# Kernel tuning notes

Hardware: AMD Instinct MI355X
Metric: run time of the kernel (lower is better)

The kernel has to match this reference:

```python
import jax, jax.numpy as jnp
import numpy as np


def _gen_grid(h, w, stride=1):
    """Normalized spherical sampling grid, shape (3*H', 3*W', 2) with (x, y) order,
    matching gen_grid_coordinates in the torch source (vectorized)."""
    pi = np.pi
    dphi = pi / h
    dth = 2 * pi / w
    t = np.tan(dth)
    p = np.tan(dphi)
    sp = p / np.cos(dth)
    # xys[kr, kc] = (x, y) tangent-plane offsets of the 3x3 kernel taps
    xys = np.array([[[-t, sp], [0.0, p], [t, sp]],
                    [[-t, 0.0], [1.0, 1.0], [t, 0.0]],
                    [[-t, -sp], [0.0, -p], [t, -sp]]], dtype=np.float64)
    X = xys[..., 0]
    Y = xys[..., 1]
    rho = np.sqrt(X ** 2 + Y ** 2)           # [3,3], nonzero everywhere
    v = np.arctan(rho)
    rr = np.arange(0, h, stride)
    cc = np.arange(0, w, stride)
    phi = -((rr + 0.5) / h * pi - pi / 2)    # [H']
    theta = (cc + 0.5) / w * 2 * pi - pi     # [W']
    sphi = np.sin(phi)[:, None, None, None]  # [H',1,1,1]
    cphi = np.cos(phi)[:, None, None, None]
    arg = np.cos(v) * sphi + Y * np.sin(v) * cphi / rho  # [H',1,3,3]
    new_phi = np.arcsin(np.clip(arg, -1.0, 1.0))
    new_theta = theta[None, :, None, None] + np.arctan(
        X * np.sin(v) / (rho * cphi * np.cos(v) - Y * sphi * np.sin(v)))  # [H',W',3,3]
    new_r = np.broadcast_to((-new_phi + pi / 2) * h / pi - 0.5, new_theta.shape).copy()
    new_c = (new_theta + pi) * w / (2 * pi) - 0.5
    new_c = (new_c + w) % w
    # center tap samples the pixel itself
    new_r[:, :, 1, 1] = rr[:, None]
    new_c[:, :, 1, 1] = cc[None, :]
    gx = new_c * 2 / w - 1
    gy = new_r * 2 / h - 1
    grid = np.stack([gx, gy], axis=-1)                     # [H',W',3,3,2]
    Hp, Wp = len(rr), len(cc)
    grid = grid.transpose(0, 2, 1, 3, 4).reshape(Hp * 3, Wp * 3, 2)
    return grid.astype(np.float32)


def _grid_sample_bilinear_zeros(x, grid):
    """torch grid_sample(mode='bilinear', padding_mode='zeros', align_corners=False).
    x: [N,C,H,W]; grid: [Hg,Wg,2] (shared over batch). Returns [N,C,Hg,Wg]."""
    N, C, H, W = x.shape
    ix = ((grid[..., 0] + 1) * W - 1) * 0.5
    iy = ((grid[..., 1] + 1) * H - 1) * 0.5
    x0 = jnp.floor(ix)
    y0 = jnp.floor(iy)
    x1 = x0 + 1
    y1 = y0 + 1
    wx1 = ix - x0
    wx0 = 1.0 - wx1
    wy1 = iy - y0
    wy0 = 1.0 - wy1

    def gather(yy, xx):
        valid = ((xx >= 0) & (xx <= W - 1) & (yy >= 0) & (yy <= H - 1)).astype(x.dtype)
        xi = jnp.clip(xx, 0, W - 1).astype(jnp.int32)
        yi = jnp.clip(yy, 0, H - 1).astype(jnp.int32)
        return x[:, :, yi, xi], valid  # [N,C,Hg,Wg], [Hg,Wg]

    v00, m00 = gather(y0, x0)
    v01, m01 = gather(y0, x1)
    v10, m10 = gather(y1, x0)
    v11, m11 = gather(y1, x1)
    return (v00 * (wy0 * wx0 * m00) + v01 * (wy0 * wx1 * m01)
            + v10 * (wy1 * wx0 * m10) + v11 * (wy1 * wx1 * m11))


def setup_inputs() -> dict:
    key = jax.random.key(0)
    k1, k2, k3 = jax.random.split(key, 3)
    N, Cin, H, W = 4, 64, 128, 256
    Cout = 128
    x = jax.random.normal(k1, (N, Cin, H, W), dtype=jnp.float32)
    fan_in = Cin * 9
    bound = 1.0 / np.sqrt(fan_in)
    weight = jax.random.uniform(k2, (Cout, Cin, 3, 3), dtype=jnp.float32,
                                minval=-bound, maxval=bound)
    bias = jnp.zeros((Cout,), dtype=jnp.float32)
    return {"x": x, "weight": weight, "bias": bias}


def reference(x, weight, bias):
    H, W = int(x.shape[2]), int(x.shape[3])
    grid = jnp.asarray(_gen_grid(H, W, 1))              # [3H, 3W, 2]
    s = _grid_sample_bilinear_zeros(x, grid)            # [N, Cin, 3H, 3W]
    y = jax.lax.conv_general_dilated(
        s, weight, window_strides=(3, 3), padding='VALID',
        dimension_numbers=('NCHW', 'OIHW', 'NCHW'))     # [N, Cout, H, W]
    return y + bias[None, :, None, None]
```

## Files before the change

### kernel.cpp

```cpp
#include <hip/hip_runtime.h>
#include <math.h>

typedef __attribute__((ext_vector_type(8))) short short8;
typedef __attribute__((ext_vector_type(8))) _Float16 half8;
typedef __attribute__((ext_vector_type(4))) _Float16 half4;
typedef __attribute__((ext_vector_type(2))) _Float16 half2;
typedef __attribute__((ext_vector_type(4))) float floatx4;
typedef __attribute__((ext_vector_type(4))) unsigned int uintx4;

#define NB    4
#define CIN   64
#define COUT  128
#define IMH   128
#define IMW   256
#define KTOT  576
#define NPIX  (IMH * IMW)
#define PXT   128
#define NDPB  (PXT * 9)
#define ROWS  4
#define CSTW  6
#define NCOL  257
#define RSTW  (NCOL * CSTW)
#define SLSTR 104
#define KCH   96

__device__ __forceinline__ unsigned pkrtz2(float a, float b) {
  unsigned r;
  asm("v_cvt_pkrtz_f16_f32 %0, %1, %2" : "=v"(r) : "v"(a), "v"(b));
  return r;
}
__device__ __forceinline__ half4 dup4(unsigned u) {
  half2 h; __builtin_memcpy(&h, &u, 4);
  return __builtin_shufflevector(h, h, 0, 1, 0, 1);
}

__global__ __launch_bounds__(256) void prep_w_kernel(const float* __restrict__ w,
                                                     unsigned short* __restrict__ wbf) {
  int idx = blockIdx.x * 256 + threadIdx.x;
  if (idx >= COUT * 8 * KCH) return;
  int co = idx / (8 * KCH);
  int K2 = idx - co * (8 * KCH);
  int cb = K2 / KCH, kk = K2 - cb * KCH;
  unsigned short v = 0;
  if (kk < 72) {
    int t = kk >> 3, chl = kk & 7;
    int ci = cb * 8 + chl;
    _Float16 h = (_Float16)w[co * KTOT + ci * 9 + t];
    __builtin_memcpy(&v, &h, 2);
  }
  wbf[(K2 >> 3) * (COUT * 8) + co * 8 + (K2 & 7)] = v;
}

__global__ __launch_bounds__(512, 4) void sphconv_kernel(
    const float* __restrict__ x, const unsigned short* __restrict__ wbf,
    const float* __restrict__ bias, float* __restrict__ out) {
  __shared__ __align__(16) unsigned int stg[ROWS * RSTW];
  __shared__ __align__(16) unsigned short Sl[PXT * SLSTR];
  __shared__ double tapA[9];
  __shared__ float  tapWy[9][2];
  __shared__ int    tapRo[9][2];

  const int tid  = threadIdx.x;
  const int lane = tid & 63;
  const int wv   = tid >> 6;
  const int lin = blockIdx.x + 2 * blockIdx.y;
  const int sw  = (lin & 7) * 32 + (lin >> 3);
  const int ct  = sw >> 7;
  const int r   = sw & 127;
  const int n   = blockIdx.z;
  const int c0  = ct * PXT;
  const int co_base = (wv & 1) * 64;
  const int px_base = (wv >> 1) * 32;
  const int rlo  = min(max(r - 2, 0), IMH - ROWS);
  const int sp  = tid & 3;
  const int scg = (tid >> 2) & 63;
  const int srr = tid >> 8;

  const float* xn = x + (size_t)n * CIN * NPIX;

  floatx4 nx[4];
  #pragma unroll
  for (int c = 0; c < 2; c++)
    #pragma unroll
    for (int rw = 0; rw < 2; rw++)
      nx[c * 2 + rw] = *(const floatx4*)(xn + (size_t)(sp * 2 + c) * NPIX
                                         + (size_t)(rlo + srr * 2 + rw) * IMW + scg * 4);

  {
    int myk = -1;
    if (lane == 0) myk = wv;
    if (wv == 0 && lane == 32) myk = 8;
    if (myk >= 0) {
      const double pi = 3.14159265358979323846;
      double dphi = pi / IMH;
      double dth  = 2.0 * pi / IMW;
      double t  = tan(dth);
      double p  = tan(dphi);
      double sp_ = p / cos(dth);
      double phi  = -(((double)r + 0.5) / IMH * pi - pi * 0.5);
      double sphi = sin(phi), cphi = cos(phi);
      int i = myk / 3, j = myk % 3;
      double atv, new_r;
      if (myk == 4) {
        atv = 0.0; new_r = (double)r;
      } else {
        double X = (j == 0) ? -t : ((j == 2) ? t : 0.0);
        double Y = 0.0;
        if (i == 0)      Y = (j == 1) ?  p :  sp_;
        else if (i == 2) Y = (j == 1) ? -p : -sp_;
        double rho = sqrt(X * X + Y * Y);
        double v   = atan(rho);
        double sv = sin(v), cv = cos(v);
        double arg = cv * sphi + Y * sv * cphi / rho;
        arg = fmin(1.0, fmax(-1.0, arg));
        double new_phi = asin(arg);
        double denom = rho * cphi * cv - Y * sphi * sv;
        atv = atan(X * sv / denom);
        new_r = (-new_phi + pi * 0.5) * IMH / pi - 0.5;
      }
      float gy = (float)(new_r * 2.0 / IMH - 1.0);
      float iy = ((gy + 1.0f) * (float)IMH - 1.0f) * 0.5f;
      float fy = floorf(iy); int y0 = (int)fy;
      float wy1 = iy - fy, wy0 = 1.0f - wy1;
      int y1 = y0 + 1;
      bool vy0 = (y0 >= 0) & (y0 <= IMH - 1);
      bool vy1 = (y1 >= 0) & (y1 <= IMH - 1);
      int y0c = min(max(y0, 0), IMH - 1), y1c = min(max(y1, 0), IMH - 1);
      int rt = min(max(y0c - rlo, 0), ROWS - 1);
      int rb = min(max(y1c - rlo, 0), ROWS - 1);
      tapA[myk] = atv;
      tapWy[myk][0] = vy0 ? wy0 : 0.0f;
      tapWy[myk][1] = vy1 ? wy1 : 0.0f;
      tapRo[myk][0] = rt * RSTW;
      tapRo[myk][1] = rb * RSTW;
    }
  }
  __syncthreads();

  int opk[3] = {0, 0, 0}, slw[3] = {0, 0, 0};
  unsigned uq0[3] = {0,0,0}, uq1[3] = {0,0,0}, uq2[3] = {0,0,0}, uq3[3] = {0,0,0};
  {
    const double pi = 3.14159265358979323846;
    #pragma unroll
    for (int dd = 0; dd < 3; dd++) {
      if (dd < 2 || tid < NDPB - 1024) {
        int d  = tid + dd * 512;
        int px = d & (PXT - 1), k = d >> 7;
        int c  = c0 + px;
        double nc;
        if (k == 4) {
          nc = (double)c;
        } else {
          double theta = ((double)c + 0.5) / IMW * (2.0 * pi) - pi;
          double new_theta = theta + tapA[k];
          nc = (new_theta + pi) * IMW / (2.0 * pi) - 0.5;
          nc = fmod(nc + (double)IMW, (double)IMW);
        }
        float gx = (float)(nc * 2.0 / IMW - 1.0);
        float ix = ((gx + 1.0f) * (float)IMW - 1.0f) * 0.5f;
        float fx = floorf(ix); int x0 = (int)fx;
        float wx1 = ix - fx, wx0 = 1.0f - wx1;
        int x1 = x0 + 1;
        int x0c = max(x0, 0);
        float w_lo = (x0 >= 0) ? wx0 : wx1;
        float w_hi = (x0 >= 0) ? ((x1 <= IMW - 1) ? wx1 : 0.0f) : 0.0f;
        float wy0m = tapWy[k][0], wy1m = tapWy[k][1];
        float w0 = wy0m * w_lo, w1 = wy0m * w_hi;
        float w2 = wy1m * w_lo, w3 = wy1m * w_hi;
        int sh0 = ((x0c >> 4) & 1) * 2;
        int sh1 = (((x0c + 1) >> 4) & 1) * 2;
        int dc  = CSTW + sh1 - sh0;
        int offt = tapRo[k][0] + x0c * CSTW + sh0;
        int offb = tapRo[k][1] + x0c * CSTW + sh0;
        opk[dd] = offt | (offb << 16);
        slw[dd] = (px * (SLSTR / 2) + k * 4) | (dc << 16);
        uq0[dd] = pkrtz2(w0, w0); uq1[dd] = pkrtz2(w1, w1);
        uq2[dd] = pkrtz2(w2, w2); uq3[dd] = pkrtz2(w3, w3);
      }
    }
  }

  #pragma unroll
  for (int rw = 0; rw < 2; rw++)
    #pragma unroll
    for (int i = 0; i < 4; i++) {
      int col = scg * 4 + i;
      int sh = ((col >> 4) & 1) * 2;
      stg[(srr * 2 + rw) * RSTW + col * CSTW + sh + sp] =
          pkrtz2(nx[rw][i], nx[2 + rw][i]);
    }
  if (tid < 16) stg[(tid >> 2) * RSTW + 256 * CSTW + (tid & 3)] = 0u;
  #pragma unroll
  for (int z = 0; z < 3; z++) {
    int q = tid + z * 512;
    int px = q / 12;
    ((unsigned int*)Sl)[px * 52 + 36 + (q - px * 12)] = 0u;
  }

  floatx4 acc[4][2];
  #pragma unroll
  for (int mt = 0; mt < 4; mt++)
    #pragma unroll
    for (int nt = 0; nt < 2; nt++)
      acc[mt][nt] = (floatx4){0.f, 0.f, 0.f, 0.f};

  __syncthreads();

  #pragma unroll 1
  for (int cb = 0; cb < 8; cb++) {
    if (cb < 7) {
      #pragma unroll
      for (int c = 0; c < 2; c++)
        #pragma unroll
        for (int rw = 0; rw < 2; rw++)
          nx[c * 2 + rw] = *(const floatx4*)(xn + (size_t)((cb + 1) * 8 + sp * 2 + c) * NPIX
                                             + (size_t)(rlo + srr * 2 + rw) * IMW + scg * 4);
    }
    #pragma unroll
    for (int dd = 0; dd < 3; dd++) {
      if (dd < 2 || tid < NDPB - 1024) {
        unsigned op = (unsigned)opk[dd];
        const unsigned* pt = stg + (op & 0xFFFFu);
        const unsigned* pb = stg + (op >> 16);
        int dc = slw[dd] >> 16;
        half4 t0  = *(const half4*)(pt);
        half4 t0h = *(const half4*)(pt + 2);
        half4 t1  = *(const half4*)(pt + dc);
        half4 t1h = *(const half4*)(pt + dc + 2);
        half4 b0  = *(const half4*)(pb);
        half4 b0h = *(const half4*)(pb + 2);
        half4 b1  = *(const half4*)(pb + dc);
        half4 b1h = *(const half4*)(pb + dc + 2);
        half4 W0 = dup4(uq0[dd]), W1 = dup4(uq1[dd]);
        half4 W2 = dup4(uq2[dd]), W3 = dup4(uq3[dd]);
        half4 slo = t0 * W0 + t1 * W1 + b0 * W2 + b1 * W3;
        half4 shi = t0h * W0 + t1h * W1 + b0h * W2 + b1h * W3;
        union { half4 h; unsigned u[2]; } ua, ub;
        ua.h = slo; ub.h = shi;
        uintx4 U = {ua.u[0], ua.u[1], ub.u[0], ub.u[1]};
        *(uintx4*)((unsigned int*)Sl + (slw[dd] & 0xFFFF)) = U;
      }
    }
    __syncthreads();
    if (cb < 7) {
      #pragma unroll
      for (int rw = 0; rw < 2; rw++)
        #pragma unroll
        for (int i = 0; i < 4; i++) {
          int col = scg * 4 + i;
          int sh = ((col >> 4) & 1) * 2;
          stg[(srr * 2 + rw) * RSTW + col * CSTW + sh + sp] =
              pkrtz2(nx[rw][i], nx[2 + rw][i]);
        }
    }
    __builtin_amdgcn_s_setprio(1);
    #pragma unroll
    for (int ks = 0; ks < 3; ks++) {
      const unsigned short* arow =
          wbf + (size_t)((cb * 12 + ks * 4 + (lane >> 4)) * COUT + co_base + (lane & 15)) * 8;
      #pragma unroll
      for (int nt = 0; nt < 2; nt++) {
        half8 b = *(const half8*)&Sl[(px_base + nt * 16 + (lane & 15)) * SLSTR
                                     + ks * 32 + (lane >> 4) * 8];
        #pragma unroll
        for (int mt = 0; mt < 4; mt++) {
          half8 a = *(const half8*)(arow + mt * 16 * 8);
          acc[mt][nt] = __builtin_amdgcn_mfma_f32_16x16x32_f16(a, b, acc[mt][nt], 0, 0, 0);
        }
      }
    }
    __builtin_amdgcn_s_setprio(0);
    __syncthreads();
  }

  #pragma unroll
  for (int mt = 0; mt < 4; mt++)
    #pragma unroll
    for (int nt = 0; nt < 2; nt++)
      #pragma unroll
      for (int rg = 0; rg < 4; rg++) {
        const int co = co_base + mt * 16 + (lane >> 4) * 4 + rg;
        const int cc = c0 + px_base + nt * 16 + (lane & 15);
        out[(((size_t)n * COUT + co) * IMH + r) * IMW + cc] = acc[mt][nt][rg] + bias[co];
      }
}

extern "C" void kernel_launch(void* const* d_in, const int* in_sizes, int n_in,
                              void* d_out, int out_size, void* d_ws, size_t ws_size,
                              hipStream_t stream) {
  const float* x    = (const float*)d_in[0];
  const float* w    = (const float*)d_in[1];
  const float* bias = (const float*)d_in[2];
  float* out = (float*)d_out;
  unsigned short* wbf = (unsigned short*)d_ws;
  (void)in_sizes; (void)n_in; (void)out_size; (void)ws_size;

  hipLaunchKernelGGL(prep_w_kernel, dim3((COUT * 8 * KCH + 255) / 256), dim3(256), 0, stream, w, wbf);
  hipLaunchKernelGGL(sphconv_kernel, dim3(IMW / PXT, IMH, NB), dim3(512), 0, stream,
                     x, wbf, bias, out);
}
```

Before: 146.0 us.

## Build MFMA B-fragments in registers from per-lane sampling descriptors, double-buffer staging

Each lane now builds its bilinear-sampled B operand directly in registers from precomputed per-tap descriptors kept in registers. This removes the Sl shared-memory round trip and one barrier per channel block. The input staging buffer is double-buffered so the next block's tile can be written while the current one is still being read. In exchange, each wave of a pixel group (waves 2g and 2g+1, which take the two output-channel halves) now does the same sampling itself, so the sampling ALU work doubles. There is also more register pressure from the six descriptor records held per lane.

```diff
diff --git a/kernel.cpp b/kernel.cpp
--- a/kernel.cpp
+++ b/kernel.cpp
@@ -1,7 +1,6 @@
 #include <hip/hip_runtime.h>
 #include <math.h>
 
-typedef __attribute__((ext_vector_type(8))) short short8;
 typedef __attribute__((ext_vector_type(8))) _Float16 half8;
 typedef __attribute__((ext_vector_type(4))) _Float16 half4;
 typedef __attribute__((ext_vector_type(2))) _Float16 half2;
@@ -21,7 +20,6 @@
 #define CSTW  6
 #define NCOL  257
 #define RSTW  (NCOL * CSTW)
-#define SLSTR 104
 #define KCH   96
 
 __device__ __forceinline__ unsigned pkrtz2(float a, float b) {
@@ -29,9 +27,13 @@
   asm("v_cvt_pkrtz_f16_f32 %0, %1, %2" : "=v"(r) : "v"(a), "v"(b));
   return r;
 }
-__device__ __forceinline__ half4 dup4(unsigned u) {
+__device__ __forceinline__ half4 bcl(unsigned u) {
   half2 h; __builtin_memcpy(&h, &u, 4);
-  return __builtin_shufflevector(h, h, 0, 1, 0, 1);
+  return __builtin_shufflevector(h, h, 0, 0, 0, 0);
+}
+__device__ __forceinline__ half4 bch(unsigned u) {
+  half2 h; __builtin_memcpy(&h, &u, 4);
+  return __builtin_shufflevector(h, h, 1, 1, 1, 1);
 }
 
 __global__ __launch_bounds__(256) void prep_w_kernel(const float* __restrict__ w,
@@ -54,8 +56,8 @@
 __global__ __launch_bounds__(512, 4) void sphconv_kernel(
     const float* __restrict__ x, const unsigned short* __restrict__ wbf,
     const float* __restrict__ bias, float* __restrict__ out) {
-  __shared__ __align__(16) unsigned int stg[ROWS * RSTW];
-  __shared__ __align__(16) unsigned short Sl[PXT * SLSTR];
+  __shared__ __align__(16) unsigned int stg[2][ROWS * RSTW];
+  __shared__ __align__(16) unsigned int descL[NDPB * 4];
   __shared__ double tapA[9];
   __shared__ float  tapWy[9][2];
   __shared__ int    tapRo[9][2];
@@ -72,6 +74,8 @@
   const int co_base = (wv & 1) * 64;
   const int px_base = (wv >> 1) * 32;
   const int rlo  = min(max(r - 2, 0), IMH - ROWS);
+  const int q    = lane >> 4;
+  const int p    = lane & 15;
   const int sp  = tid & 3;
   const int scg = (tid >> 2) & 63;
   const int srr = tid >> 8;
@@ -95,8 +99,8 @@
       double dphi = pi / IMH;
       double dth  = 2.0 * pi / IMW;
       double t  = tan(dth);
-      double p  = tan(dphi);
-      double sp_ = p / cos(dth);
+      double pp = tan(dphi);
+      double sp_ = pp / cos(dth);
       double phi  = -(((double)r + 0.5) / IMH * pi - pi * 0.5);
       double sphi = sin(phi), cphi = cos(phi);
       int i = myk / 3, j = myk % 3;
@@ -106,8 +110,8 @@
       } else {
         double X = (j == 0) ? -t : ((j == 2) ? t : 0.0);
         double Y = 0.0;
-        if (i == 0)      Y = (j == 1) ?  p :  sp_;
-        else if (i == 2) Y = (j == 1) ? -p : -sp_;
+        if (i == 0)      Y = (j == 1) ?  pp :  sp_;
+        else if (i == 2) Y = (j == 1) ? -pp : -sp_;
         double rho = sqrt(X * X + Y * Y);
         double v   = atan(rho);
         double sv = sin(v), cv = cos(v);
@@ -137,8 +141,6 @@
   }
   __syncthreads();
 
-  int opk[3] = {0, 0, 0}, slw[3] = {0, 0, 0};
-  unsigned uq0[3] = {0,0,0}, uq1[3] = {0,0,0}, uq2[3] = {0,0,0}, uq3[3] = {0,0,0};
   {
     const double pi = 3.14159265358979323846;
     #pragma unroll
@@ -165,17 +167,17 @@
         float w_lo = (x0 >= 0) ? wx0 : wx1;
         float w_hi = (x0 >= 0) ? ((x1 <= IMW - 1) ? wx1 : 0.0f) : 0.0f;
         float wy0m = tapWy[k][0], wy1m = tapWy[k][1];
-        float w0 = wy0m * w_lo, w1 = wy0m * w_hi;
-        float w2 = wy1m * w_lo, w3 = wy1m * w_hi;
         int sh0 = ((x0c >> 4) & 1) * 2;
         int sh1 = (((x0c + 1) >> 4) & 1) * 2;
         int dc  = CSTW + sh1 - sh0;
         int offt = tapRo[k][0] + x0c * CSTW + sh0;
         int offb = tapRo[k][1] + x0c * CSTW + sh0;
-        opk[dd] = offt | (offb << 16);
-        slw[dd] = (px * (SLSTR / 2) + k * 4) | (dc << 16);
-        uq0[dd] = pkrtz2(w0, w0); uq1[dd] = pkrtz2(w1, w1);
-        uq2[dd] = pkrtz2(w2, w2); uq3[dd] = pkrtz2(w3, w3);
+        uintx4 rec;
+        rec.x = (unsigned)(offt | (offb << 16));
+        rec.y = pkrtz2(wy0m * w_lo, wy0m * w_hi);
+        rec.z = pkrtz2(wy1m * w_lo, wy1m * w_hi);
+        rec.w = (unsigned)dc;
+        *(uintx4*)&descL[(px * 9 + k) * 4] = rec;
       }
     }
   }
@@ -186,16 +188,23 @@
     for (int i = 0; i < 4; i++) {
       int col = scg * 4 + i;
       int sh = ((col >> 4) & 1) * 2;
-      stg[(srr * 2 + rw) * RSTW + col * CSTW + sh + sp] =
+      stg[0][(srr * 2 + rw) * RSTW + col * CSTW + sh + sp] =
           pkrtz2(nx[rw][i], nx[2 + rw][i]);
     }
-  if (tid < 16) stg[(tid >> 2) * RSTW + 256 * CSTW + (tid & 3)] = 0u;
-  #pragma unroll
-  for (int z = 0; z < 3; z++) {
-    int q = tid + z * 512;
-    int px = q / 12;
-    ((unsigned int*)Sl)[px * 52 + 36 + (q - px * 12)] = 0u;
-  }
+  if (tid < 32) stg[tid >> 4][((tid >> 2) & 3) * RSTW + 256 * CSTW + (tid & 3)] = 0u;
+
+  __syncthreads();
+
+  uintx4 R[6];
+  #pragma unroll
+  for (int nt = 0; nt < 2; nt++)
+    #pragma unroll
+    for (int j = 0; j < 3; j++) {
+      int tap = q + j * 4;
+      int px  = px_base + nt * 16 + p;
+      if (tap < 9) R[nt * 3 + j] = *(const uintx4*)&descL[(px * 9 + tap) * 4];
+      else         R[nt * 3 + j] = (uintx4){0u, 0u, 0u, (unsigned)CSTW};
+    }
 
   floatx4 acc[4][2];
   #pragma unroll
@@ -203,8 +212,6 @@
     #pragma unroll
     for (int nt = 0; nt < 2; nt++)
       acc[mt][nt] = (floatx4){0.f, 0.f, 0.f, 0.f};
-
-  __syncthreads();
 
   #pragma unroll 1
   for (int cb = 0; cb < 8; cb++) {
@@ -216,13 +223,16 @@
           nx[c * 2 + rw] = *(const floatx4*)(xn + (size_t)((cb + 1) * 8 + sp * 2 + c) * NPIX
                                              + (size_t)(rlo + srr * 2 + rw) * IMW + scg * 4);
     }
-    #pragma unroll
-    for (int dd = 0; dd < 3; dd++) {
-      if (dd < 2 || tid < NDPB - 1024) {
-        unsigned op = (unsigned)opk[dd];
-        const unsigned* pt = stg + (op & 0xFFFFu);
-        const unsigned* pb = stg + (op >> 16);
-        int dc = slw[dd] >> 16;
+    const unsigned int* sb = &stg[cb & 1][0];
+    #pragma unroll
+    for (int nt = 0; nt < 2; nt++) {
+      #pragma unroll
+      for (int ks = 0; ks < 3; ks++) {
+        uintx4 rec = R[nt * 3 + ks];
+        unsigned op = rec.x;
+        int dc = (int)rec.w;
+        const unsigned int* pt = sb + (op & 0xFFFFu);
+        const unsigned int* pb = sb + (op >> 16);
         half4 t0  = *(const half4*)(pt);
         half4 t0h = *(const half4*)(pt + 2);
         half4 t1  = *(const half4*)(pt + dc);
@@ -231,17 +241,22 @@
         half4 b0h = *(const half4*)(pb + 2);
         half4 b1  = *(const half4*)(pb + dc);
         half4 b1h = *(const half4*)(pb + dc + 2);
-        half4 W0 = dup4(uq0[dd]), W1 = dup4(uq1[dd]);
-        half4 W2 = dup4(uq2[dd]), W3 = dup4(uq3[dd]);
+        half4 W0 = bcl(rec.y), W1 = bch(rec.y);
+        half4 W2 = bcl(rec.z), W3 = bch(rec.z);
         half4 slo = t0 * W0 + t1 * W1 + b0 * W2 + b1 * W3;
         half4 shi = t0h * W0 + t1h * W1 + b0h * W2 + b1h * W3;
-        union { half4 h; unsigned u[2]; } ua, ub;
-        ua.h = slo; ub.h = shi;
-        uintx4 U = {ua.u[0], ua.u[1], ub.u[0], ub.u[1]};
-        *(uintx4*)((unsigned int*)Sl + (slw[dd] & 0xFFFF)) = U;
-      }
-    }
-    __syncthreads();
+        half8 b = __builtin_shufflevector(slo, shi, 0, 1, 2, 3, 4, 5, 6, 7);
+        const unsigned short* arow =
+            wbf + (size_t)((cb * 12 + ks * 4 + q) * COUT + co_base + p) * 8;
+        __builtin_amdgcn_s_setprio(1);
+        #pragma unroll
+        for (int mt = 0; mt < 4; mt++) {
+          half8 a = *(const half8*)(arow + mt * 16 * 8);
+          acc[mt][nt] = __builtin_amdgcn_mfma_f32_16x16x32_f16(a, b, acc[mt][nt], 0, 0, 0);
+        }
+        __builtin_amdgcn_s_setprio(0);
+      }
+    }
     if (cb < 7) {
       #pragma unroll
       for (int rw = 0; rw < 2; rw++)
@@ -249,27 +264,10 @@
         for (int i = 0; i < 4; i++) {
           int col = scg * 4 + i;
           int sh = ((col >> 4) & 1) * 2;
-          stg[(srr * 2 + rw) * RSTW + col * CSTW + sh + sp] =
+          stg[(cb + 1) & 1][(srr * 2 + rw) * RSTW + col * CSTW + sh + sp] =
               pkrtz2(nx[rw][i], nx[2 + rw][i]);
         }
     }
-    __builtin_amdgcn_s_setprio(1);
-    #pragma unroll
-    for (int ks = 0; ks < 3; ks++) {
-      const unsigned short* arow =
-          wbf + (size_t)((cb * 12 + ks * 4 + (lane >> 4)) * COUT + co_base + (lane & 15)) * 8;
-      #pragma unroll
-      for (int nt = 0; nt < 2; nt++) {
-        half8 b = *(const half8*)&Sl[(px_base + nt * 16 + (lane & 15)) * SLSTR
-                                     + ks * 32 + (lane >> 4) * 8];
-        #pragma unroll
-        for (int mt = 0; mt < 4; mt++) {
-          half8 a = *(const half8*)(arow + mt * 16 * 8);
-          acc[mt][nt] = __builtin_amdgcn_mfma_f32_16x16x32_f16(a, b, acc[mt][nt], 0, 0, 0);
-        }
-      }
-    }
-    __builtin_amdgcn_s_setprio(0);
     __syncthreads();
   }
 
@@ -279,8 +277,8 @@
     for (int nt = 0; nt < 2; nt++)
       #pragma unroll
       for (int rg = 0; rg < 4; rg++) {
-        const int co = co_base + mt * 16 + (lane >> 4) * 4 + rg;
-        const int cc = c0 + px_base + nt * 16 + (lane & 15);
+        const int co = co_base + mt * 16 + q * 4 + rg;
+        const int cc = c0 + px_base + nt * 16 + p;
         out[(((size_t)n * COUT + co) * IMH + r) * IMW + cc] = acc[mt][nt][rg] + bias[co];
       }
 }
```

Result: slower. 244.6 us (+67.5%).
